# Optimization experiments

Hardware: AMD Instinct MI355X
Metric: run time of the kernel (lower is better)

The kernel has to match this reference:

```python
import jax, jax.numpy as jnp
import numpy as np

B, S, D, H, E = 4, 1024, 1024, 4096, 8


def setup_inputs() -> dict:
    key = jax.random.key(0)
    ks = jax.random.split(key, 5)
    sd = 1.0 / np.sqrt(D)
    sh = 1.0 / np.sqrt(H)
    x = jax.random.normal(ks[0], (B, S, D), dtype=jnp.float32)
    # stacked expert weights: Linear(D->H), ReLU, Linear(H->D)
    W1 = jax.random.normal(ks[1], (E, D, H), dtype=jnp.float32) * sd
    b1 = jnp.zeros((E, H), dtype=jnp.float32)
    W2 = jax.random.normal(ks[2], (E, H, D), dtype=jnp.float32) * sh
    b2 = jnp.zeros((E, D), dtype=jnp.float32)
    # gate Linear(D->E)
    Wg = jax.random.normal(ks[3], (D, E), dtype=jnp.float32) * sd
    bg = jnp.zeros((E,), dtype=jnp.float32)
    return {"x": x, "W1": W1, "b1": b1, "W2": W2, "b2": b2,
            "Wg": Wg, "bg": bg, "top_k": 2}


def reference(x, W1, b1, W2, b2, Wg, bg, top_k):
    # gating
    gating_scores = jnp.einsum('bsd,de->bse', x, Wg) + bg          # [B,S,E]
    gating_probs = jax.nn.softmax(gating_scores, axis=-1)
    _, top_k_indices = jax.lax.top_k(gating_probs, top_k)          # [B,S,K]
    n_exp = Wg.shape[1]
    # per-token 0/1 mask of selected experts (matches torch sum over k of mask)
    # NOTE: original code multiplies by the binary mask only; top_k_probs are
    # computed but NOT used as combine weights. We reproduce that faithfully.
    sel = jnp.sum(top_k_indices[..., None] == jnp.arange(n_exp), axis=2)  # [B,S,E]
    sel = sel.astype(x.dtype)
    # dense all-experts FFN (as the original does)
    h = jax.nn.relu(jnp.einsum('bsd,edh->bseh', x, W1) + b1)       # [B,S,E,H]
    eo = jnp.einsum('bseh,ehd->bsed', h, W2) + b2                  # [B,S,E,D]
    output = jnp.einsum('bsed,bse->bsd', eo, sel)                  # [B,S,D]
    return (output, gating_scores)
```

## Files before the change

### kernel.cpp

```cpp
#include <hip/hip_runtime.h>
#include <hip/hip_bf16.h>
#include <stdint.h>

#define B_ 4
#define S_ 1024
#define D_ 1024
#define H_ 4096
#define E_ 8
#define T_ (B_*S_)

#define GBM 128
#define BK 64
#define MAXT1 2432
#define MAXT2 1280
#define T1BLK 8192
#define T2BLK 8192

typedef __bf16 bf16x8 __attribute__((ext_vector_type(8)));
typedef float f32x4 __attribute__((ext_vector_type(4)));
typedef unsigned short ushort8 __attribute__((ext_vector_type(8)));
typedef unsigned short ushort4v __attribute__((ext_vector_type(4)));

__device__ __forceinline__ unsigned short f2bf(float f) {
  union { float f; uint32_t u; } v; v.f = f;
  uint32_t u = v.u;
  u += 0x7fff + ((u >> 16) & 1);
  return (unsigned short)(u >> 16);
}

__device__ __forceinline__ void gl16(const void* g, void* l) {
  __builtin_amdgcn_global_load_lds(
      (const __attribute__((address_space(1))) void*)g,
      (__attribute__((address_space(3))) void*)l,
      16, 0, 0);
}

__device__ __forceinline__ void transpose_tile(
    const float* __restrict__ in, unsigned short* __restrict__ outp,
    int R, int C, int e, int r0, int c0, int t,
    unsigned short (*tile)[66]) {
  const size_t eoff = (size_t)e * R * C;
  {
    const int r = t >> 2, cseg = (t & 3) * 16;
    const float4* s4 = (const float4*)(in + eoff + (size_t)(r0 + r) * C + (c0 + cseg));
    float4 v0 = s4[0], v1 = s4[1], v2 = s4[2], v3 = s4[3];
    ushort8 w0, w1;
    w0[0]=f2bf(v0.x); w0[1]=f2bf(v0.y); w0[2]=f2bf(v0.z); w0[3]=f2bf(v0.w);
    w0[4]=f2bf(v1.x); w0[5]=f2bf(v1.y); w0[6]=f2bf(v1.z); w0[7]=f2bf(v1.w);
    w1[0]=f2bf(v2.x); w1[1]=f2bf(v2.y); w1[2]=f2bf(v2.z); w1[3]=f2bf(v2.w);
    w1[4]=f2bf(v3.x); w1[5]=f2bf(v3.y); w1[6]=f2bf(v3.z); w1[7]=f2bf(v3.w);
    *(ushort8*)&tile[r][cseg]     = w0;
    *(ushort8*)&tile[r][cseg + 8] = w1;
  }
  __syncthreads();
  {
    const int c = t >> 2, rseg = (t & 3) * 16;
    ushort8 w0, w1;
#pragma unroll
    for (int j = 0; j < 8; ++j) {
      w0[j] = tile[rseg + j][c];
      w1[j] = tile[rseg + 8 + j][c];
    }
    unsigned short* dst = outp + eoff + (size_t)(c0 + c) * R + (r0 + rseg);
    *(ushort8*)dst       = w0;
    *(ushort8*)(dst + 8) = w1;
  }
}

__global__ __launch_bounds__(256) void transpose_conv(
    const float* __restrict__ in, unsigned short* __restrict__ outp,
    int R, int C) {
  __shared__ unsigned short tile[64][66];
  transpose_tile(in, outp, R, C, blockIdx.z, blockIdx.y * 64, blockIdx.x * 64,
                 threadIdx.x, tile);
}

__global__ __launch_bounds__(256) void gate_t1_kernel(
    const float* __restrict__ x, const float* __restrict__ Wg,
    const float* __restrict__ bg, float* __restrict__ scores,
    unsigned short* __restrict__ xb,
    int* __restrict__ cnt, int* __restrict__ lists,
    const float* __restrict__ W1, unsigned short* __restrict__ WT1) {
  __shared__ unsigned short tile[64][66];
  if (blockIdx.x >= T_ / 4) {
    int bid = blockIdx.x - T_ / 4;
    int e = bid >> 10, rem = bid & 1023;
    int cx = rem & 63, ry = rem >> 6;
    transpose_tile(W1, WT1, D_, H_, e, ry * 64, cx * 64, threadIdx.x, tile);
    return;
  }
  int t = blockIdx.x * 4 + (threadIdx.x >> 6);
  int l = threadIdx.x & 63;
  float acc[E_];
#pragma unroll
  for (int e = 0; e < E_; ++e) acc[e] = 0.f;
  const float* xr = x + (size_t)t * D_;
  unsigned short* xbr = xb + (size_t)t * D_;
  for (int k4 = l * 4; k4 < D_; k4 += 256) {
    float4 xv = *(const float4*)(xr + k4);
    ushort4v wq;
    wq[0] = f2bf(xv.x); wq[1] = f2bf(xv.y); wq[2] = f2bf(xv.z); wq[3] = f2bf(xv.w);
    *(ushort4v*)(xbr + k4) = wq;
#pragma unroll
    for (int q = 0; q < 4; ++q) {
      float xs = (q == 0) ? xv.x : (q == 1) ? xv.y : (q == 2) ? xv.z : xv.w;
      const float4* w = (const float4*)(Wg + (size_t)(k4 + q) * E_);
      float4 w0 = w[0], w1 = w[1];
      acc[0] += xs * w0.x; acc[1] += xs * w0.y; acc[2] += xs * w0.z; acc[3] += xs * w0.w;
      acc[4] += xs * w1.x; acc[5] += xs * w1.y; acc[6] += xs * w1.z; acc[7] += xs * w1.w;
    }
  }
#pragma unroll
  for (int off = 32; off > 0; off >>= 1)
#pragma unroll
    for (int e = 0; e < E_; ++e) acc[e] += __shfl_xor(acc[e], off, 64);
  if (l == 0) {
    float s[E_];
#pragma unroll
    for (int e = 0; e < E_; ++e) {
      s[e] = acc[e] + bg[e];
      scores[(size_t)t * E_ + e] = s[e];
    }
    int i1 = 0; float m1 = -1e30f;
#pragma unroll
    for (int e = 0; e < E_; ++e) if (s[e] > m1) { m1 = s[e]; i1 = e; }
    int i2 = -1; float m2 = -1e30f;
#pragma unroll
    for (int e = 0; e < E_; ++e) if (e != i1 && s[e] > m2) { m2 = s[e]; i2 = e; }
    int p1 = atomicAdd(&cnt[i1], 1); lists[i1 * T_ + p1] = t;
    int p2 = atomicAdd(&cnt[i2], 1); lists[i2 * T_ + p2] = t;
  }
}

__global__ void scan_kernel(const int* __restrict__ cnt, int* __restrict__ off,
                            int* __restrict__ hdr, int* __restrict__ t1tab,
                            int* __restrict__ t2tab) {
  int mt[E_], offl[E_];
  int o = 0;
  for (int e = 0; e < E_; ++e) {
    offl[e] = o; o += cnt[e];
    mt[e] = (cnt[e] + GBM - 1) / GBM;
  }
  const int t = threadIdx.x;
  {
    int e = t >> 5, nt = t & 31;
    int s1 = 0;
    for (int q = 0; q < e; ++q) s1 += mt[q] * (H_ / GBM);
    int base = s1 + nt * mt[e];
    for (int m = 0; m < mt[e]; ++m) t1tab[base + m] = (e << 16) | (m << 8) | nt;
  }
  if (t < 128) {
    int e = t >> 4, idx = t & 15, sp = idx >> 3, nt = idx & 7;
    int s2 = 0;
    for (int q = 0; q < e; ++q) s2 += mt[q] * 2 * (D_ / GBM);
    int base = s2 + (sp * (D_ / GBM) + nt) * mt[e];
    for (int m = 0; m < mt[e]; ++m)
      t2tab[base + m] = (e << 16) | (m << 8) | (sp << 6) | nt;
  }
  if (t == 0) {
    int s1 = 0, s2 = 0;
    for (int e = 0; e < E_; ++e) {
      s1 += mt[e] * (H_ / GBM); s2 += mt[e] * 2 * (D_ / GBM);
      off[e] = offl[e];
    }
    hdr[0] = s1; hdr[1] = s2;
  }
}

template <int LAYER, int SPLITK, bool FUSET2>
__global__ __launch_bounds__(256, 4) void ffn_gemm(
    const unsigned short* __restrict__ xb,
    const unsigned short* __restrict__ hbuf,
    const unsigned short* __restrict__ WT,
    const float* __restrict__ bias,
    const int* __restrict__ cnt, const int* __restrict__ off,
    const int* __restrict__ lists,
    const int* __restrict__ tab, const int* __restrict__ hdr,
    unsigned short* __restrict__ hout,
    float* __restrict__ out,
    const float* __restrict__ Wsrc, unsigned short* __restrict__ WTdst)
{
  constexpr int K = (LAYER == 1) ? D_ : H_;
  constexpr int N = (LAYER == 1) ? H_ : D_;
  constexpr int KS = K / SPLITK;
  constexpr int NT = KS / BK;

  __shared__ unsigned short sA[GBM * BK];
  __shared__ unsigned short sB[GBM * BK];

  if (FUSET2 && blockIdx.x >= MAXT1) {
    int bid = blockIdx.x - MAXT1;
    int e = bid >> 10, rem = bid & 1023;
    int cx = rem & 15, ry = rem >> 4;
    transpose_tile(Wsrc, WTdst, H_, D_, e, ry * 64, cx * 64, threadIdx.x,
                   (unsigned short (*)[66])sA);
    return;
  }

  const int ntask = hdr[LAYER - 1];
  const int b = blockIdx.x;
  if (b >= ntask) return;
  const int q = ntask >> 3, r = ntask & 7;
  const int x = b & 7, ii = b >> 3;
  const int task = (x < r ? x * (q + 1) : r * (q + 1) + (x - r) * q) + ii;

  const int ent = tab[task];
  const int e  = ent >> 16;
  const int m0 = ((ent >> 8) & 0xff) * GBM;
  const int sp = (ent >> 6) & 3;
  const int n0 = (ent & 63) * GBM;
  const int k0 = sp * KS;
  const int count = cnt[e];
  const int oe = off[e];
  const int* lst = lists + e * T_;

  const int tid  = threadIdx.x;
  const int lane = tid & 63;
  const int wv   = tid >> 6;
  const int wm   = (wv >> 1) * 64;
  const int wn   = (wv & 1) * 64;

  const int srow   = lane >> 3;
  const int schunk = (lane & 7) * 16;
  const int sgoff  = schunk ^ (srow << 4);

  const char* arow[4];
  const char* brow[4];
#pragma unroll
  for (int i = 0; i < 4; ++i) {
    int rr = i * 32 + wv * 8 + srow;
    int gr = m0 + rr;
    if (LAYER == 1) {
      int tok = (gr < count) ? lst[gr] : lst[m0];
      arow[i] = (const char*)(xb + (size_t)tok * K + k0);
    } else {
      int r2 = (gr < count) ? gr : m0;
      arow[i] = (const char*)(hbuf + (size_t)(oe + r2) * K + k0);
    }
    brow[i] = (const char*)(WT + (size_t)e * N * K + (size_t)(n0 + rr) * K + k0);
  }

  const int lrow = lane & 15;
  const int kg   = lane >> 4;
  const int fswz = (lrow & 7) << 4;

  f32x4 acc[4][4];
#pragma unroll
  for (int i = 0; i < 4; ++i)
#pragma unroll
    for (int j = 0; j < 4; ++j) acc[i][j] = (f32x4){0.f, 0.f, 0.f, 0.f};

#pragma unroll 1
  for (int t = 0; t < NT; ++t) {
    const int kb = t * 128;
#pragma unroll
    for (int i = 0; i < 4; ++i)
      gl16(arow[i] + kb + sgoff, (char*)sA + (i * 32 + wv * 8) * 128);
#pragma unroll
    for (int i = 0; i < 4; ++i)
      gl16(brow[i] + kb + sgoff, (char*)sB + (i * 32 + wv * 8) * 128);
    __syncthreads();
#pragma unroll
    for (int ks = 0; ks < 2; ++ks) {
      bf16x8 af[4], bfm[4];
      const int kbyte = ks * 64 + kg * 16;
#pragma unroll
      for (int i = 0; i < 4; ++i) {
        af[i]  = *(const bf16x8*)((const char*)sA + (wm + i * 16 + lrow) * 128 + (kbyte ^ fswz));
        bfm[i] = *(const bf16x8*)((const char*)sB + (wn + i * 16 + lrow) * 128 + (kbyte ^ fswz));
      }
#pragma unroll
      for (int i = 0; i < 4; ++i)
#pragma unroll
        for (int j = 0; j < 4; ++j)
          acc[i][j] = __builtin_amdgcn_mfma_f32_16x16x32_bf16(af[i], bfm[j], acc[i][j], 0, 0, 0);
    }
    __syncthreads();
  }

  const int rbase = 4 * kg;
#pragma unroll
  for (int i = 0; i < 4; ++i) {
#pragma unroll
    for (int r2 = 0; r2 < 4; ++r2) {
      int row  = wm + i * 16 + rbase + r2;
      int grow = m0 + row;
      if (grow < count) {
#pragma unroll
        for (int j = 0; j < 4; ++j) {
          int col  = wn + j * 16 + lrow;
          int gcol = n0 + col;
          float bv = (SPLITK == 1 || sp == 0) ? bias[(size_t)e * N + gcol] : 0.f;
          float v = acc[i][j][r2] + bv;
          if (LAYER == 1) {
            v = v > 0.f ? v : 0.f;
            hout[(size_t)(oe + grow) * H_ + gcol] = f2bf(v);
          } else {
            int tok = lst[grow];
            atomicAdd(&out[(size_t)tok * D_ + gcol], v);
          }
        }
      }
    }
  }
}

extern "C" void kernel_launch(void* const* d_in, const int* in_sizes, int n_in,
                              void* d_out, int out_size, void* d_ws, size_t ws_size,
                              hipStream_t stream) {
  (void)in_sizes; (void)n_in; (void)out_size;
  const float* x  = (const float*)d_in[0];
  const float* W1 = (const float*)d_in[1];
  const float* b1 = (const float*)d_in[2];
  const float* W2 = (const float*)d_in[3];
  const float* b2 = (const float*)d_in[4];
  const float* Wg = (const float*)d_in[5];
  const float* bg = (const float*)d_in[6];

  float* out    = (float*)d_out;
  float* scores = out + (size_t)T_ * D_;

  char* ws = (char*)d_ws;
  int* cnt   = (int*)ws;
  int* off   = (int*)(ws + 32);
  int* hdr   = (int*)(ws + 64);
  int* t1tab = (int*)(ws + 128);
  int* t2tab = (int*)(ws + 10240);
  int* lists = (int*)(ws + 16384);
  const size_t BASE = 16384 + 131072;
  unsigned short* xb   = (unsigned short*)(ws + BASE);
  unsigned short* hbuf = (unsigned short*)(ws + BASE + 8388608);
  unsigned short* WT1  = (unsigned short*)(ws + BASE + 8388608 + 67108864);
  const size_t NEED2 = BASE + 8388608 + 67108864ull * 3;
  const bool fuse = (ws_size >= NEED2);
  unsigned short* WT2 = fuse ? (WT1 + 67108864 / 2) : WT1;

  hipMemsetAsync(out, 0, (size_t)T_ * D_ * sizeof(float), stream);
  hipMemsetAsync(cnt, 0, 64, stream);

  gate_t1_kernel<<<T_ / 4 + T1BLK, 256, 0, stream>>>(
      x, Wg, bg, scores, xb, cnt, lists, W1, WT1);
  scan_kernel<<<1, 256, 0, stream>>>(cnt, off, hdr, t1tab, t2tab);

  if (fuse) {
    ffn_gemm<1, 1, true><<<MAXT1 + T2BLK, 256, 0, stream>>>(
        xb, hbuf, WT1, b1, cnt, off, lists, t1tab, hdr, hbuf, nullptr, W2, WT2);
  } else {
    ffn_gemm<1, 1, false><<<MAXT1, 256, 0, stream>>>(
        xb, hbuf, WT1, b1, cnt, off, lists, t1tab, hdr, hbuf, nullptr, nullptr, nullptr);
    transpose_conv<<<dim3(D_ / 64, H_ / 64, E_), 256, 0, stream>>>(W2, WT2, H_, D_);
  }

  ffn_gemm<2, 2, false><<<MAXT2, 256, 0, stream>>>(
      xb, hbuf, WT2, b2, cnt, off, lists, t2tab, hdr, nullptr, out, nullptr, nullptr);
}
```

Baseline: 411.3 us.

## Enlarge MoE GEMM tiles to 256x256 with double-buffered LDS pipeline

Grows each GEMM block tile from 128x128 to 256x256, run by 512-thread blocks where each wave owns a 128x64 sub-tile. Global-to-LDS loads are double-buffered so the next K slice streams in while MFMAs run on the current one, with one barrier per iteration and raised wave priority around the MFMA burst. Layer 2 moves to split-K of 4, and the scan and task tables are rebuilt for the new tile counts. The aim is more operand reuse per loaded byte and less exposed load latency, at the cost of higher register and LDS use, one block per CU, and more atomic adds in layer 2.

```diff
diff --git a/kernel.cpp b/kernel.cpp
--- a/kernel.cpp
+++ b/kernel.cpp
@@ -9,10 +9,10 @@
 #define E_ 8
 #define T_ (B_*S_)
 
-#define GBM 128
+#define GBM 256
 #define BK 64
-#define MAXT1 2432
-#define MAXT2 1280
+#define MAXT1 640
+#define MAXT2 640
 #define T1BLK 8192
 #define T2BLK 8192
 
@@ -34,6 +34,7 @@
       (__attribute__((address_space(3))) void*)l,
       16, 0, 0);
 }
+#define MEMFENCE asm volatile("" ::: "memory")
 
 __device__ __forceinline__ void transpose_tile(
     const float* __restrict__ in, unsigned short* __restrict__ outp,
@@ -142,25 +143,25 @@
     mt[e] = (cnt[e] + GBM - 1) / GBM;
   }
   const int t = threadIdx.x;
-  {
-    int e = t >> 5, nt = t & 31;
+  if (t < 128) {
+    int e = t >> 4, nt = t & 15;
     int s1 = 0;
     for (int q = 0; q < e; ++q) s1 += mt[q] * (H_ / GBM);
     int base = s1 + nt * mt[e];
     for (int m = 0; m < mt[e]; ++m) t1tab[base + m] = (e << 16) | (m << 8) | nt;
-  }
-  if (t < 128) {
-    int e = t >> 4, idx = t & 15, sp = idx >> 3, nt = idx & 7;
+  } else {
+    int t2 = t - 128;
+    int e = t2 >> 4, idx = t2 & 15, sp = idx >> 2, nt = idx & 3;
     int s2 = 0;
-    for (int q = 0; q < e; ++q) s2 += mt[q] * 2 * (D_ / GBM);
+    for (int q = 0; q < e; ++q) s2 += mt[q] * 4 * (D_ / GBM);
     int base = s2 + (sp * (D_ / GBM) + nt) * mt[e];
     for (int m = 0; m < mt[e]; ++m)
-      t2tab[base + m] = (e << 16) | (m << 8) | (sp << 6) | nt;
+      t2tab[base + m] = (e << 16) | (m << 8) | (sp << 4) | nt;
   }
   if (t == 0) {
     int s1 = 0, s2 = 0;
     for (int e = 0; e < E_; ++e) {
-      s1 += mt[e] * (H_ / GBM); s2 += mt[e] * 2 * (D_ / GBM);
+      s1 += mt[e] * (H_ / GBM); s2 += mt[e] * 4 * (D_ / GBM);
       off[e] = offl[e];
     }
     hdr[0] = s1; hdr[1] = s2;
@@ -168,7 +169,7 @@
 }
 
 template <int LAYER, int SPLITK, bool FUSET2>
-__global__ __launch_bounds__(256, 4) void ffn_gemm(
+__global__ __launch_bounds__(512, 1) void ffn_gemm(
     const unsigned short* __restrict__ xb,
     const unsigned short* __restrict__ hbuf,
     const unsigned short* __restrict__ WT,
@@ -185,15 +186,16 @@
   constexpr int KS = K / SPLITK;
   constexpr int NT = KS / BK;
 
-  __shared__ unsigned short sA[GBM * BK];
-  __shared__ unsigned short sB[GBM * BK];
+  __shared__ unsigned short sA[2][GBM * BK];
+  __shared__ unsigned short sB[2][GBM * BK];
 
   if (FUSET2 && blockIdx.x >= MAXT1) {
-    int bid = blockIdx.x - MAXT1;
+    int bid = (blockIdx.x - MAXT1) * 2 + (threadIdx.x >> 8);
     int e = bid >> 10, rem = bid & 1023;
     int cx = rem & 15, ry = rem >> 4;
-    transpose_tile(Wsrc, WTdst, H_, D_, e, ry * 64, cx * 64, threadIdx.x,
-                   (unsigned short (*)[66])sA);
+    transpose_tile(Wsrc, WTdst, H_, D_, e, ry * 64, cx * 64, threadIdx.x & 255,
+                   (unsigned short (*)[66])((char*)&sA[0][0] +
+                                            (threadIdx.x >> 8) * 16384));
     return;
   }
 
@@ -207,8 +209,8 @@
   const int ent = tab[task];
   const int e  = ent >> 16;
   const int m0 = ((ent >> 8) & 0xff) * GBM;
-  const int sp = (ent >> 6) & 3;
-  const int n0 = (ent & 63) * GBM;
+  const int sp = (ent >> 4) & 3;
+  const int n0 = (ent & 15) * GBM;
   const int k0 = sp * KS;
   const int count = cnt[e];
   const int oe = off[e];
@@ -217,8 +219,8 @@
   const int tid  = threadIdx.x;
   const int lane = tid & 63;
   const int wv   = tid >> 6;
-  const int wm   = (wv >> 1) * 64;
-  const int wn   = (wv & 1) * 64;
+  const int wm   = (wv >> 2) * 128;
+  const int wn   = (wv & 3) * 64;
 
   const int srow   = lane >> 3;
   const int schunk = (lane & 7) * 16;
@@ -228,7 +230,7 @@
   const char* brow[4];
 #pragma unroll
   for (int i = 0; i < 4; ++i) {
-    int rr = i * 32 + wv * 8 + srow;
+    int rr = i * 64 + wv * 8 + srow;
     int gr = m0 + rr;
     if (LAYER == 1) {
       int tok = (gr < count) ? lst[gr] : lst[m0];
@@ -240,47 +242,69 @@
     brow[i] = (const char*)(WT + (size_t)e * N * K + (size_t)(n0 + rr) * K + k0);
   }
 
+  auto stage = [&](int buf, int t) {
+    const int kb = t * 128;
+#pragma unroll
+    for (int i = 0; i < 4; ++i)
+      gl16(arow[i] + kb + sgoff, (char*)&sA[buf][0] + (i * 64 + wv * 8) * 128);
+#pragma unroll
+    for (int i = 0; i < 4; ++i)
+      gl16(brow[i] + kb + sgoff, (char*)&sB[buf][0] + (i * 64 + wv * 8) * 128);
+  };
+
   const int lrow = lane & 15;
   const int kg   = lane >> 4;
   const int fswz = (lrow & 7) << 4;
 
-  f32x4 acc[4][4];
-#pragma unroll
-  for (int i = 0; i < 4; ++i)
+  f32x4 acc[8][4];
+#pragma unroll
+  for (int i = 0; i < 8; ++i)
 #pragma unroll
     for (int j = 0; j < 4; ++j) acc[i][j] = (f32x4){0.f, 0.f, 0.f, 0.f};
+
+  stage(0, 0);
+  asm volatile("s_waitcnt vmcnt(0)" ::: "memory");
+  MEMFENCE;
+  __builtin_amdgcn_s_barrier();
+  MEMFENCE;
 
 #pragma unroll 1
   for (int t = 0; t < NT; ++t) {
-    const int kb = t * 128;
-#pragma unroll
-    for (int i = 0; i < 4; ++i)
-      gl16(arow[i] + kb + sgoff, (char*)sA + (i * 32 + wv * 8) * 128);
-#pragma unroll
-    for (int i = 0; i < 4; ++i)
-      gl16(brow[i] + kb + sgoff, (char*)sB + (i * 32 + wv * 8) * 128);
-    __syncthreads();
-#pragma unroll
-    for (int ks = 0; ks < 2; ++ks) {
-      bf16x8 af[4], bfm[4];
-      const int kbyte = ks * 64 + kg * 16;
-#pragma unroll
-      for (int i = 0; i < 4; ++i) {
-        af[i]  = *(const bf16x8*)((const char*)sA + (wm + i * 16 + lrow) * 128 + (kbyte ^ fswz));
-        bfm[i] = *(const bf16x8*)((const char*)sB + (wn + i * 16 + lrow) * 128 + (kbyte ^ fswz));
-      }
-#pragma unroll
-      for (int i = 0; i < 4; ++i)
+    const int buf = t & 1;
+    if (t + 1 < NT) stage(buf ^ 1, t + 1);
+    bf16x8 af[8][2], bfm[4][2];
+#pragma unroll
+    for (int i = 0; i < 8; ++i) {
+      const int ra = wm + i * 16 + lrow;
+#pragma unroll
+      for (int ks = 0; ks < 2; ++ks)
+        af[i][ks] = *(const bf16x8*)((const char*)&sA[buf][0] + ra * 128 + ((ks * 64 + kg * 16) ^ fswz));
+    }
+#pragma unroll
+    for (int j = 0; j < 4; ++j) {
+      const int rb = wn + j * 16 + lrow;
+#pragma unroll
+      for (int ks = 0; ks < 2; ++ks)
+        bfm[j][ks] = *(const bf16x8*)((const char*)&sB[buf][0] + rb * 128 + ((ks * 64 + kg * 16) ^ fswz));
+    }
+    __builtin_amdgcn_s_setprio(1);
+#pragma unroll
+    for (int ks = 0; ks < 2; ++ks)
+#pragma unroll
+      for (int i = 0; i < 8; ++i)
 #pragma unroll
         for (int j = 0; j < 4; ++j)
-          acc[i][j] = __builtin_amdgcn_mfma_f32_16x16x32_bf16(af[i], bfm[j], acc[i][j], 0, 0, 0);
-    }
-    __syncthreads();
+          acc[i][j] = __builtin_amdgcn_mfma_f32_16x16x32_bf16(af[i][ks], bfm[j][ks], acc[i][j], 0, 0, 0);
+    __builtin_amdgcn_s_setprio(0);
+    if (t + 1 < NT) { asm volatile("s_waitcnt vmcnt(0)" ::: "memory"); }
+    MEMFENCE;
+    __builtin_amdgcn_s_barrier();
+    MEMFENCE;
   }
 
   const int rbase = 4 * kg;
 #pragma unroll
-  for (int i = 0; i < 4; ++i) {
+  for (int i = 0; i < 8; ++i) {
 #pragma unroll
     for (int r2 = 0; r2 < 4; ++r2) {
       int row  = wm + i * 16 + rbase + r2;
@@ -325,7 +349,7 @@
   int* off   = (int*)(ws + 32);
   int* hdr   = (int*)(ws + 64);
   int* t1tab = (int*)(ws + 128);
-  int* t2tab = (int*)(ws + 10240);
+  int* t2tab = (int*)(ws + 128 + 4 * MAXT1);
   int* lists = (int*)(ws + 16384);
   const size_t BASE = 16384 + 131072;
   unsigned short* xb   = (unsigned short*)(ws + BASE);
@@ -343,14 +367,14 @@
   scan_kernel<<<1, 256, 0, stream>>>(cnt, off, hdr, t1tab, t2tab);
 
   if (fuse) {
-    ffn_gemm<1, 1, true><<<MAXT1 + T2BLK, 256, 0, stream>>>(
+    ffn_gemm<1, 1, true><<<MAXT1 + T2BLK / 2, 512, 0, stream>>>(
         xb, hbuf, WT1, b1, cnt, off, lists, t1tab, hdr, hbuf, nullptr, W2, WT2);
   } else {
-    ffn_gemm<1, 1, false><<<MAXT1, 256, 0, stream>>>(
+    ffn_gemm<1, 1, false><<<MAXT1, 512, 0, stream>>>(
         xb, hbuf, WT1, b1, cnt, off, lists, t1tab, hdr, hbuf, nullptr, nullptr, nullptr);
     transpose_conv<<<dim3(D_ / 64, H_ / 64, E_), 256, 0, stream>>>(W2, WT2, H_, D_);
   }
 
-  ffn_gemm<2, 2, false><<<MAXT2, 256, 0, stream>>>(
+  ffn_gemm<2, 4, false><<<MAXT2, 512, 0, stream>>>(
       xb, hbuf, WT2, b2, cnt, off, lists, t2tab, hdr, nullptr, out, nullptr, nullptr);
 }
```

Measured after the change: 534.4 us. +29.9%, slower.

## Widen layer-1 GEMM tile to 128x256 and split into dedicated kernels

Applied to the files above, without the earlier changes.

The first expert GEMM now uses a 128x256 output tile per block, with each wave computing 64x128 and holding 4x8 MFMA accumulators. This halves the number of layer-1 tasks and raises the arithmetic intensity of each LDS load. The layer-2 GEMM moves into its own kernel, and the scan and task-table logic are updated to match. In exchange it uses more registers and LDS, launch bounds drop to 2 blocks per SM, and fewer blocks are available to fill the GPU.

```diff
diff --git a/kernel.cpp b/kernel.cpp
--- a/kernel.cpp
+++ b/kernel.cpp
@@ -9,10 +9,9 @@
 #define E_ 8
 #define T_ (B_*S_)
 
-#define GBM 128
 #define BK 64
-#define MAXT1 2432
-#define MAXT2 1280
+#define MAXT1 1152
+#define MAXT2 1152
 #define T1BLK 8192
 #define T2BLK 8192
 
@@ -139,65 +138,175 @@
   int o = 0;
   for (int e = 0; e < E_; ++e) {
     offl[e] = o; o += cnt[e];
-    mt[e] = (cnt[e] + GBM - 1) / GBM;
+    mt[e] = (cnt[e] + 127) / 128;
   }
   const int t = threadIdx.x;
-  {
-    int e = t >> 5, nt = t & 31;
+  if (t < 128) {
+    int e = t >> 4, nt = t & 15;
     int s1 = 0;
-    for (int q = 0; q < e; ++q) s1 += mt[q] * (H_ / GBM);
+    for (int q = 0; q < e; ++q) s1 += mt[q] * 16;
     int base = s1 + nt * mt[e];
     for (int m = 0; m < mt[e]; ++m) t1tab[base + m] = (e << 16) | (m << 8) | nt;
-  }
-  if (t < 128) {
-    int e = t >> 4, idx = t & 15, sp = idx >> 3, nt = idx & 7;
+  } else {
+    int t2 = t - 128;
+    int e = t2 >> 4, idx = t2 & 15, sp = idx >> 3, nt = idx & 7;
     int s2 = 0;
-    for (int q = 0; q < e; ++q) s2 += mt[q] * 2 * (D_ / GBM);
-    int base = s2 + (sp * (D_ / GBM) + nt) * mt[e];
+    for (int q = 0; q < e; ++q) s2 += mt[q] * 16;
+    int base = s2 + (sp * 8 + nt) * mt[e];
     for (int m = 0; m < mt[e]; ++m)
       t2tab[base + m] = (e << 16) | (m << 8) | (sp << 6) | nt;
   }
   if (t == 0) {
-    int s1 = 0, s2 = 0;
-    for (int e = 0; e < E_; ++e) {
-      s1 += mt[e] * (H_ / GBM); s2 += mt[e] * 2 * (D_ / GBM);
-      off[e] = offl[e];
-    }
-    hdr[0] = s1; hdr[1] = s2;
-  }
-}
-
-template <int LAYER, int SPLITK, bool FUSET2>
-__global__ __launch_bounds__(256, 4) void ffn_gemm(
+    int s = 0;
+    for (int e = 0; e < E_; ++e) { s += mt[e] * 16; off[e] = offl[e]; }
+    hdr[0] = s; hdr[1] = s;
+  }
+}
+
+template <bool FUSET2>
+__global__ __launch_bounds__(256, 2) void ffn_gemm1(
     const unsigned short* __restrict__ xb,
+    const unsigned short* __restrict__ WT,
+    const float* __restrict__ bias,
+    const int* __restrict__ cnt, const int* __restrict__ off,
+    const int* __restrict__ lists,
+    const int* __restrict__ tab, const int* __restrict__ hdr,
+    unsigned short* __restrict__ hout,
+    const float* __restrict__ Wsrc, unsigned short* __restrict__ WTdst)
+{
+  constexpr int K = D_;
+  constexpr int N = H_;
+  constexpr int NT = K / BK;
+
+  __shared__ unsigned short sA[128 * BK];
+  __shared__ unsigned short sB[256 * BK];
+
+  if (FUSET2 && blockIdx.x >= MAXT1) {
+    int bid = blockIdx.x - MAXT1;
+    int e = bid >> 10, rem = bid & 1023;
+    int cx = rem & 15, ry = rem >> 4;
+    transpose_tile(Wsrc, WTdst, H_, D_, e, ry * 64, cx * 64, threadIdx.x,
+                   (unsigned short (*)[66])sB);
+    return;
+  }
+
+  const int ntask = hdr[0];
+  const int b = blockIdx.x;
+  if (b >= ntask) return;
+  const int q = ntask >> 3, r = ntask & 7;
+  const int x = b & 7, ii = b >> 3;
+  const int task = (x < r ? x * (q + 1) : r * (q + 1) + (x - r) * q) + ii;
+
+  const int ent = tab[task];
+  const int e  = ent >> 16;
+  const int m0 = ((ent >> 8) & 0xff) * 128;
+  const int n0 = (ent & 63) * 256;
+  const int count = cnt[e];
+  const int oe = off[e];
+  const int* lst = lists + e * T_;
+
+  const int tid  = threadIdx.x;
+  const int lane = tid & 63;
+  const int wv   = tid >> 6;
+  const int wm   = (wv >> 1) * 64;
+  const int wn   = (wv & 1) * 128;
+
+  const int srow   = lane >> 3;
+  const int schunk = (lane & 7) * 16;
+  const int sgoff  = schunk ^ (srow << 4);
+
+  const char* arow[4];
+  const char* brow[8];
+#pragma unroll
+  for (int i = 0; i < 4; ++i) {
+    int rr = i * 32 + wv * 8 + srow;
+    int gr = m0 + rr;
+    int tok = (gr < count) ? lst[gr] : lst[m0];
+    arow[i] = (const char*)(xb + (size_t)tok * K);
+  }
+#pragma unroll
+  for (int i = 0; i < 8; ++i) {
+    int rr = i * 32 + wv * 8 + srow;
+    brow[i] = (const char*)(WT + (size_t)e * N * K + (size_t)(n0 + rr) * K);
+  }
+
+  const int lrow = lane & 15;
+  const int kg   = lane >> 4;
+  const int fswz = (lrow & 7) << 4;
+
+  f32x4 acc[4][8];
+#pragma unroll
+  for (int i = 0; i < 4; ++i)
+#pragma unroll
+    for (int j = 0; j < 8; ++j) acc[i][j] = (f32x4){0.f, 0.f, 0.f, 0.f};
+
+#pragma unroll 1
+  for (int t = 0; t < NT; ++t) {
+    const int kb = t * 128;
+#pragma unroll
+    for (int i = 0; i < 4; ++i)
+      gl16(arow[i] + kb + sgoff, (char*)sA + (i * 32 + wv * 8) * 128);
+#pragma unroll
+    for (int i = 0; i < 8; ++i)
+      gl16(brow[i] + kb + sgoff, (char*)sB + (i * 32 + wv * 8) * 128);
+    __syncthreads();
+#pragma unroll
+    for (int ks = 0; ks < 2; ++ks) {
+      bf16x8 af[4], bfm[8];
+      const int kbyte = ks * 64 + kg * 16;
+#pragma unroll
+      for (int i = 0; i < 4; ++i)
+        af[i] = *(const bf16x8*)((const char*)sA + (wm + i * 16 + lrow) * 128 + (kbyte ^ fswz));
+#pragma unroll
+      for (int j = 0; j < 8; ++j)
+        bfm[j] = *(const bf16x8*)((const char*)sB + (wn + j * 16 + lrow) * 128 + (kbyte ^ fswz));
+#pragma unroll
+      for (int i = 0; i < 4; ++i)
+#pragma unroll
+        for (int j = 0; j < 8; ++j)
+          acc[i][j] = __builtin_amdgcn_mfma_f32_16x16x32_bf16(af[i], bfm[j], acc[i][j], 0, 0, 0);
+    }
+    __syncthreads();
+  }
+
+  const int rbase = 4 * kg;
+#pragma unroll
+  for (int i = 0; i < 4; ++i) {
+#pragma unroll
+    for (int r2 = 0; r2 < 4; ++r2) {
+      int row  = wm + i * 16 + rbase + r2;
+      int grow = m0 + row;
+      if (grow < count) {
+#pragma unroll
+        for (int j = 0; j < 8; ++j) {
+          int gcol = n0 + wn + j * 16 + lrow;
+          float v = acc[i][j][r2] + bias[(size_t)e * N + gcol];
+          v = v > 0.f ? v : 0.f;
+          hout[(size_t)(oe + grow) * H_ + gcol] = f2bf(v);
+        }
+      }
+    }
+  }
+}
+
+__global__ __launch_bounds__(256, 4) void ffn_gemm2(
     const unsigned short* __restrict__ hbuf,
     const unsigned short* __restrict__ WT,
     const float* __restrict__ bias,
     const int* __restrict__ cnt, const int* __restrict__ off,
     const int* __restrict__ lists,
     const int* __restrict__ tab, const int* __restrict__ hdr,
-    unsigned short* __restrict__ hout,
-    float* __restrict__ out,
-    const float* __restrict__ Wsrc, unsigned short* __restrict__ WTdst)
+    float* __restrict__ out)
 {
-  constexpr int K = (LAYER == 1) ? D_ : H_;
-  constexpr int N = (LAYER == 1) ? H_ : D_;
-  constexpr int KS = K / SPLITK;
+  constexpr int K = H_;
+  constexpr int N = D_;
+  constexpr int KS = K / 2;
   constexpr int NT = KS / BK;
 
-  __shared__ unsigned short sA[GBM * BK];
-  __shared__ unsigned short sB[GBM * BK];
-
-  if (FUSET2 && blockIdx.x >= MAXT1) {
-    int bid = blockIdx.x - MAXT1;
-    int e = bid >> 10, rem = bid & 1023;
-    int cx = rem & 15, ry = rem >> 4;
-    transpose_tile(Wsrc, WTdst, H_, D_, e, ry * 64, cx * 64, threadIdx.x,
-                   (unsigned short (*)[66])sA);
-    return;
-  }
-
-  const int ntask = hdr[LAYER - 1];
+  __shared__ unsigned short sA[128 * BK];
+  __shared__ unsigned short sB[128 * BK];
+
+  const int ntask = hdr[1];
   const int b = blockIdx.x;
   if (b >= ntask) return;
   const int q = ntask >> 3, r = ntask & 7;
@@ -206,9 +315,9 @@
 
   const int ent = tab[task];
   const int e  = ent >> 16;
-  const int m0 = ((ent >> 8) & 0xff) * GBM;
+  const int m0 = ((ent >> 8) & 0xff) * 128;
   const int sp = (ent >> 6) & 3;
-  const int n0 = (ent & 63) * GBM;
+  const int n0 = (ent & 63) * 128;
   const int k0 = sp * KS;
   const int count = cnt[e];
   const int oe = off[e];
@@ -230,13 +339,8 @@
   for (int i = 0; i < 4; ++i) {
     int rr = i * 32 + wv * 8 + srow;
     int gr = m0 + rr;
-    if (LAYER == 1) {
-      int tok = (gr < count) ? lst[gr] : lst[m0];
-      arow[i] = (const char*)(xb + (size_t)tok * K + k0);
-    } else {
-      int r2 = (gr < count) ? gr : m0;
-      arow[i] = (const char*)(hbuf + (size_t)(oe + r2) * K + k0);
-    }
+    int r2 = (gr < count) ? gr : m0;
+    arow[i] = (const char*)(hbuf + (size_t)(oe + r2) * K + k0);
     brow[i] = (const char*)(WT + (size_t)e * N * K + (size_t)(n0 + rr) * K + k0);
   }
 
@@ -288,17 +392,11 @@
       if (grow < count) {
 #pragma unroll
         for (int j = 0; j < 4; ++j) {
-          int col  = wn + j * 16 + lrow;
-          int gcol = n0 + col;
-          float bv = (SPLITK == 1 || sp == 0) ? bias[(size_t)e * N + gcol] : 0.f;
+          int gcol = n0 + wn + j * 16 + lrow;
+          float bv = (sp == 0) ? bias[(size_t)e * N + gcol] : 0.f;
           float v = acc[i][j][r2] + bv;
-          if (LAYER == 1) {
-            v = v > 0.f ? v : 0.f;
-            hout[(size_t)(oe + grow) * H_ + gcol] = f2bf(v);
-          } else {
-            int tok = lst[grow];
-            atomicAdd(&out[(size_t)tok * D_ + gcol], v);
-          }
+          int tok = lst[grow];
+          atomicAdd(&out[(size_t)tok * D_ + gcol], v);
         }
       }
     }
@@ -325,7 +423,7 @@
   int* off   = (int*)(ws + 32);
   int* hdr   = (int*)(ws + 64);
   int* t1tab = (int*)(ws + 128);
-  int* t2tab = (int*)(ws + 10240);
+  int* t2tab = (int*)(ws + 128 + 4 * MAXT1);
   int* lists = (int*)(ws + 16384);
   const size_t BASE = 16384 + 131072;
   unsigned short* xb   = (unsigned short*)(ws + BASE);
@@ -343,14 +441,14 @@
   scan_kernel<<<1, 256, 0, stream>>>(cnt, off, hdr, t1tab, t2tab);
 
   if (fuse) {
-    ffn_gemm<1, 1, true><<<MAXT1 + T2BLK, 256, 0, stream>>>(
-        xb, hbuf, WT1, b1, cnt, off, lists, t1tab, hdr, hbuf, nullptr, W2, WT2);
+    ffn_gemm1<true><<<MAXT1 + T2BLK, 256, 0, stream>>>(
+        xb, WT1, b1, cnt, off, lists, t1tab, hdr, hbuf, W2, WT2);
   } else {
-    ffn_gemm<1, 1, false><<<MAXT1, 256, 0, stream>>>(
-        xb, hbuf, WT1, b1, cnt, off, lists, t1tab, hdr, hbuf, nullptr, nullptr, nullptr);
+    ffn_gemm1<false><<<MAXT1, 256, 0, stream>>>(
+        xb, WT1, b1, cnt, off, lists, t1tab, hdr, hbuf, nullptr, nullptr);
     transpose_conv<<<dim3(D_ / 64, H_ / 64, E_), 256, 0, stream>>>(W2, WT2, H_, D_);
   }
 
-  ffn_gemm<2, 2, false><<<MAXT2, 256, 0, stream>>>(
-      xb, hbuf, WT2, b2, cnt, off, lists, t2tab, hdr, nullptr, out, nullptr, nullptr);
-}
+  ffn_gemm2<<<MAXT2, 256, 0, stream>>>(
+      hbuf, WT2, b2, cnt, off, lists, t2tab, hdr, out);
+}
```

Measured after the change: 419.3 us. No clear change (+1.9%).
